# Kernel optimization log

Hardware: AMD Instinct MI355X
Metric: run time of the kernel (lower is better)

The kernel has to match this reference:

```python
import jax, jax.numpy as jnp
import numpy as np

B, L, C, D, H, EL, DFF, NC, PH = 32, 512, 64, 512, 8, 3, 2048, 8, 256
DK = D // H


def _ln(x, g, b):
    m = jnp.mean(x, -1, keepdims=True)
    v = jnp.var(x, -1, keepdims=True)
    return (x - m) / jnp.sqrt(v + 1e-5) * g + b


def _projector(x, stats, cw, w1, b1, w2, b2, w3):
    # circular Conv1d over feature axis with seq_len input channels -> 1 channel
    xp = jnp.pad(x, ((0, 0), (0, 0), (1, 1)), mode='wrap')  # [B,L,C+2]
    win = jnp.stack([xp[:, :, :-2], xp[:, :, 1:-1], xp[:, :, 2:]], -1)  # [B,L,C,3]
    y = jnp.einsum('bsck,sk->bc', win, cw)  # [B,C]
    h = jnp.concatenate([y, stats[:, 0, :]], -1)  # [B,2C]
    h = jax.nn.relu(h @ w1.T + b1)
    h = jax.nn.relu(h @ w2.T + b2)
    return h @ w3.T


def setup_inputs() -> dict:
    key = jax.random.key(0)
    ks = jax.random.split(key, 20)
    n = lambda i, shape, s=0.02: jax.random.normal(ks[i], shape, jnp.float32) * s
    return {
        'x_enc': jax.random.normal(ks[0], (B, L, C), jnp.float32),
        'emb_conv_w': n(1, (D, C, 3), 0.05),
        'tau_conv_w': n(2, (L, 3), 0.05),
        'tau_w1': n(3, (PH, 2 * C)), 'tau_b1': jnp.zeros((PH,), jnp.float32),
        'tau_w2': n(4, (PH, PH)), 'tau_b2': jnp.zeros((PH,), jnp.float32),
        'tau_w3': n(5, (1, PH)),
        'delta_conv_w': n(6, (L, 3), 0.05),
        'delta_w1': n(7, (PH, 2 * C)), 'delta_b1': jnp.zeros((PH,), jnp.float32),
        'delta_w2': n(8, (PH, PH)), 'delta_b2': jnp.zeros((PH,), jnp.float32),
        'delta_w3': n(9, (L, PH)),
        'Wq': n(10, (EL, D, D)), 'bq': jnp.zeros((EL, D), jnp.float32),
        'Wk': n(11, (EL, D, D)), 'bk': jnp.zeros((EL, D), jnp.float32),
        'Wv': n(12, (EL, D, D)), 'bv': jnp.zeros((EL, D), jnp.float32),
        'Wo': n(13, (EL, D, D)), 'bo': jnp.zeros((EL, D), jnp.float32),
        'ff_w1': n(14, (EL, DFF, D)), 'ff_b1': jnp.zeros((EL, DFF), jnp.float32),
        'ff_w2': n(15, (EL, D, DFF)), 'ff_b2': jnp.zeros((EL, D), jnp.float32),
        'ln1_g': jnp.ones((EL, D), jnp.float32), 'ln1_b': jnp.zeros((EL, D), jnp.float32),
        'ln2_g': jnp.ones((EL, D), jnp.float32), 'ln2_b': jnp.zeros((EL, D), jnp.float32),
        'norm_g': jnp.ones((D,), jnp.float32), 'norm_b': jnp.zeros((D,), jnp.float32),
        'proj_w': n(16, (NC, D * L), 0.005), 'proj_b': jnp.zeros((NC,), jnp.float32),
    }


def reference(x_enc, emb_conv_w, tau_conv_w, tau_w1, tau_b1, tau_w2, tau_b2, tau_w3,
              delta_conv_w, delta_w1, delta_b1, delta_w2, delta_b2, delta_w3,
              Wq, bq, Wk, bk, Wv, bv, Wo, bo, ff_w1, ff_b1, ff_w2, ff_b2,
              ln1_g, ln1_b, ln2_g, ln2_b, norm_g, norm_b, proj_w, proj_b):
    x_raw = jax.lax.stop_gradient(x_enc)
    mean_enc = jax.lax.stop_gradient(jnp.mean(x_enc, 1, keepdims=True))  # [B,1,C]
    std_enc = jax.lax.stop_gradient(jnp.sqrt(jnp.var(x_enc, axis=1, keepdims=True) + 1e-5))
    tau = jnp.exp(_projector(x_raw, std_enc, tau_conv_w, tau_w1, tau_b1, tau_w2, tau_b2, tau_w3))  # [B,1]
    delta = _projector(x_raw, mean_enc, delta_conv_w, delta_w1, delta_b1, delta_w2, delta_b2, delta_w3)  # [B,L]

    # TokenEmbedding: circular Conv1d (kernel 3, no bias) over time + sinusoidal PE
    xp = jnp.pad(x_enc, ((0, 0), (1, 1), (0, 0)), mode='wrap')
    win = jnp.stack([xp[:, :-2], xp[:, 1:-1], xp[:, 2:]], -1)  # [B,L,C,3]
    x = jnp.einsum('blck,dck->bld', win, emb_conv_w)
    pos = jnp.arange(L, dtype=jnp.float32)[:, None]
    div = jnp.exp(jnp.arange(0, D, 2, dtype=jnp.float32) * (-jnp.log(10000.0) / D))
    pe = jnp.zeros((L, D), jnp.float32).at[:, 0::2].set(jnp.sin(pos * div)).at[:, 1::2].set(jnp.cos(pos * div))
    x = x + pe[None]

    scale = 1.0 / jnp.sqrt(jnp.float32(DK))
    tau4 = tau[:, :, None, None]      # [B,1,1,1]
    delta4 = delta[:, None, None, :]  # [B,1,1,S]
    for i in range(EL):
        q = (x @ Wq[i].T + bq[i]).reshape(B, L, H, DK)
        k = (x @ Wk[i].T + bk[i]).reshape(B, L, H, DK)
        v = (x @ Wv[i].T + bv[i]).reshape(B, L, H, DK)
        scores = jnp.einsum('blhe,bshe->bhls', q, k) * tau4 + delta4  # DSAttention rescale/shift
        A = jax.nn.softmax(scale * scores, axis=-1)
        o = jnp.einsum('bhls,bshd->blhd', A, v).reshape(B, L, D)
        x = x + (o @ Wo[i].T + bo[i])
        x = _ln(x, ln1_g[i], ln1_b[i])
        y = jax.nn.gelu(x @ ff_w1[i].T + ff_b1[i], approximate=False)  # conv1 kernel=1 == linear
        y = y @ ff_w2[i].T + ff_b2[i]
        x = _ln(x + y, ln2_g[i], ln2_b[i])
    x = _ln(x, norm_g, norm_b)
    out = jax.nn.gelu(x, approximate=False).reshape(B, -1)
    return out @ proj_w.T + proj_b
```

## Files before the change

### kernel.cpp

```cpp
#include <hip/hip_runtime.h>
#include <hip/hip_bf16.h>
#include <math.h>

#define B_   32
#define L_   512
#define C_   64
#define D_   512
#define H_   8
#define EL_  3
#define DFF_ 2048
#define NC_  8
#define PH_  256
#define DK_  64
#define NTOK (B_*L_)

typedef unsigned short u16;
typedef unsigned int   u32;
typedef __attribute__((ext_vector_type(4))) float f32x4;
typedef __attribute__((ext_vector_type(8))) short s16x8;

__device__ __forceinline__ u16 f2b(float f){
  u32 u = __float_as_uint(f);
  u32 r = (u + 0x7fffu + ((u >> 16) & 1u)) >> 16;
  return (u16)r;
}
__device__ __forceinline__ float b2f(u16 u){ return __uint_as_float(((u32)u) << 16); }

__device__ __forceinline__ void gload16(const void* g, void* l){
  __builtin_amdgcn_global_load_lds(
      (const __attribute__((address_space(1))) u32*)g,
      (__attribute__((address_space(3))) u32*)l, 16, 0, 0);
}

__device__ __forceinline__ float gelu_exact(float x){
  return 0.5f * x * (1.f + erff(x * 0.70710678118654752f));
}


__global__ __launch_bounds__(256) void k_stats(const float* __restrict__ x,
    float* __restrict__ mean, float* __restrict__ stdv){
  int b = blockIdx.x, t = threadIdx.x;
  const float* p = x + (size_t)b*L_*C_;
  float s = 0.f, q = 0.f;
  for (int i = t; i < L_*C_; i += 256){ float v = p[i]; s += v; q += v*v; }
  __shared__ float ss[256], qq[256];
  ss[t] = s; qq[t] = q;
  __syncthreads();
  if (t < 64){
    float S = ss[t]+ss[t+64]+ss[t+128]+ss[t+192];
    float Q = qq[t]+qq[t+64]+qq[t+128]+qq[t+192];
    float m = S*(1.f/L_);
    mean[b*64+t] = m;
    stdv[b*64+t] = sqrtf(Q*(1.f/L_) - m*m + 1e-5f);
  }
}

__global__ __launch_bounds__(256) void k_mlp(const float* __restrict__ x,
    const float* __restrict__ mean, const float* __restrict__ stdv,
    const float* __restrict__ cw_t, const float* __restrict__ w1t, const float* __restrict__ b1t,
    const float* __restrict__ w2t, const float* __restrict__ b2t, const float* __restrict__ w3t,
    const float* __restrict__ cw_d, const float* __restrict__ w1d, const float* __restrict__ b1d,
    const float* __restrict__ w2d, const float* __restrict__ b2d, const float* __restrict__ w3d,
    float* __restrict__ tau, float* __restrict__ delta)
{
  int b = blockIdx.x, sel = blockIdx.y, t = threadIdx.x;
  const float* cw = sel ? cw_d : cw_t;
  const float* w1 = sel ? w1d : w1t;  const float* b1 = sel ? b1d : b1t;
  const float* w2 = sel ? w2d : w2t;  const float* b2 = sel ? b2d : b2t;
  const float* st = sel ? mean : stdv;
  __shared__ float h0[128], h1s[256], h2s[256], red[256];
  __shared__ float c4[4][64];
  {
    int c = t & 63, g = t >> 6;
    int cm = (c+63)&63, cp = (c+1)&63;
    const float* xrow = x + (size_t)b*L_*C_;
    float acc = 0.f;
    for (int s = g*128; s < (g+1)*128; ++s){
      const float* r = xrow + s*C_;
      acc += r[cm]*cw[s*3] + r[c]*cw[s*3+1] + r[cp]*cw[s*3+2];
    }
    c4[g][c] = acc;
  }
  __syncthreads();
  if (t < 64)       h0[t] = c4[0][t]+c4[1][t]+c4[2][t]+c4[3][t];
  else if (t < 128) h0[t] = st[b*64 + (t-64)];
  __syncthreads();
  { float a = b1[t]; for (int j=0;j<128;++j) a += h0[j]*w1[t*128+j]; h1s[t] = fmaxf(a,0.f); }
  __syncthreads();
  { float a = b2[t]; for (int j=0;j<256;++j) a += h1s[j]*w2[t*256+j]; h2s[t] = fmaxf(a,0.f); }
  __syncthreads();
  if (sel == 0){
    red[t] = h2s[t]*w3t[t];
    __syncthreads();
    for (int o=128;o>0;o>>=1){ if (t<o) red[t]+=red[t+o]; __syncthreads(); }
    if (t == 0) tau[b] = expf(red[0]);
  } else {
    for (int l = t; l < L_; l += 256){
      float a = 0.f;
      for (int j=0;j<256;++j) a += h2s[j]*w3d[l*256+j];
      delta[b*L_ + l] = a;
    }
  }
}

__global__ void k_pe(float* __restrict__ pe){
  int i = blockIdx.x*256 + threadIdx.x;
  if (i >= L_*D_/2) return;
  int l = i >> 8, j = i & 255;
  float div = expf((float)(2*j) * (-9.210340371976184f / (float)D_));
  float arg = (float)l * div;
  pe[l*D_ + 2*j]   = sinf(arg);
  pe[l*D_ + 2*j+1] = cosf(arg);
}

__global__ void k_awin(const float* __restrict__ x, u16* __restrict__ awin){
  int i = blockIdx.x*256 + threadIdx.x;
  if (i >= NTOK*192) return;
  int col = i % 192, row = i / 192;
  int k = col >> 6, c = col & 63;
  int b = row >> 9, l = row & 511;
  int ls = (l + k + 511) & 511;
  awin[i] = f2b(x[((size_t)((b<<9) | ls))*64 + c]);
}

__global__ void k_embw(const float* __restrict__ w, u16* __restrict__ o){
  int i = blockIdx.x*256 + threadIdx.x;
  if (i >= D_*192) return;
  int d = i / 192, col = i % 192, k = col >> 6, c = col & 63;
  o[i] = f2b(w[(d*64 + c)*3 + k]);
}

__global__ void k_packqkv(const float* __restrict__ Wq, const float* __restrict__ Wk,
                          const float* __restrict__ Wv, u16* __restrict__ o){
  int i = blockIdx.x*256 + threadIdx.x;
  if (i >= EL_*1536*D_) return;
  int e = i / (1536*D_), r = i % (1536*D_);
  int n = r / D_, k = r % D_;
  const float* src = (n < 512) ? Wq + ((size_t)e*512 + n)*512 + k
                   : (n < 1024) ? Wk + ((size_t)e*512 + (n-512))*512 + k
                                : Wv + ((size_t)e*512 + (n-1024))*512 + k;
  o[i] = f2b(*src);
}
__global__ void k_packb(const float* __restrict__ bq, const float* __restrict__ bk,
                        const float* __restrict__ bv, float* __restrict__ o){
  int i = blockIdx.x*256 + threadIdx.x;
  if (i >= EL_*1536) return;
  int e = i/1536, n = i%1536;
  o[i] = (n<512) ? bq[e*512+n] : (n<1024) ? bk[e*512+n-512] : bv[e*512+n-1024];
}

__global__ void k_f2b(const float* __restrict__ in, u16* __restrict__ out, int n){
  int i = blockIdx.x*256 + threadIdx.x;
  if (i < n) out[i] = f2b(in[i]);
}

__global__ __launch_bounds__(256,2) void k_gemm(
    const u16* __restrict__ A, const u16* __restrict__ Bm,
    int M, int N, int K,
    const float* __restrict__ bias, const float* __restrict__ pe,
    int dogelu,
    float* __restrict__ outF, u16* __restrict__ outB)
{
  __shared__ u16 As[128*64];
  __shared__ u16 Bs[128*64];
  int tid = threadIdx.x;
  int l = tid & 63, w = tid >> 6;
  int wr = w >> 1, wc = w & 1;
  int lo = l & 15, lg = l >> 4;

  int flat = blockIdx.x + gridDim.x*blockIdx.y;
  int nwg  = gridDim.x*gridDim.y;
  int n1   = ((nwg & 7) == 0) ? ((flat & 7)*(nwg >> 3) + (flat >> 3)) : flat;
  int bx   = n1 % gridDim.x, by = n1 / gridDim.x;
  int m0 = by * 128, n0 = bx * 128;

  f32x4 acc[4][4];
  #pragma unroll
  for (int m=0;m<4;++m)
    #pragma unroll
    for (int n=0;n<4;++n) acc[m][n] = (f32x4){0.f,0.f,0.f,0.f};

  int swz = lo & 7;
  int ktn = K >> 6;
  for (int kt = 0; kt < ktn; ++kt){
    #pragma unroll
    for (int i=0;i<4;++i){
      int cA = i*256 + tid;
      int row = cA >> 3, sub = (cA & 7) ^ (row & 7);
      gload16(A  + (size_t)(m0+row)*K + kt*64 + sub*8, &As[cA*8]);
      gload16(Bm + (size_t)(n0+row)*K + kt*64 + sub*8, &Bs[cA*8]);
    }
    __syncthreads();
    #pragma unroll
    for (int kk=0;kk<2;++kk){
      int cb = ((kk<<2)|lg) ^ swz;
      s16x8 af[4], bfr[4];
      #pragma unroll
      for (int m=0;m<4;++m) af[m]  = *(const s16x8*)&As[(wr*64 + m*16 + lo)*64 + cb*8];
      #pragma unroll
      for (int n=0;n<4;++n) bfr[n] = *(const s16x8*)&Bs[(wc*64 + n*16 + lo)*64 + cb*8];
      #pragma unroll
      for (int m=0;m<4;++m)
        #pragma unroll
        for (int n=0;n<4;++n)
          acc[m][n] = __builtin_amdgcn_mfma_f32_16x16x32_bf16(af[m], bfr[n], acc[m][n], 0,0,0);
    }
    __syncthreads();
  }

  #pragma unroll
  for (int m=0;m<4;++m){
    int rbase = m0 + wr*64 + m*16 + lg*4;
    #pragma unroll
    for (int n=0;n<4;++n){
      int col = n0 + wc*64 + n*16 + lo;
      float bv = bias ? bias[col] : 0.f;
      #pragma unroll
      for (int r=0;r<4;++r){
        int row = rbase + r;
        float v = acc[m][n][r] + bv;
        if (pe) v += pe[(size_t)(row & 511)*N + col];
        if (dogelu) v = gelu_exact(v);
        size_t o = (size_t)row*N + col;
        if (outF) outF[o] = v;
        if (outB) outB[o] = f2b(v);
      }
    }
  }
}

__global__ __launch_bounds__(512,2) void k_gemm256(
    const u16* __restrict__ A, const u16* __restrict__ Bm,
    int M, int N, int K,
    const float* __restrict__ bias,
    int dogelu,
    float* __restrict__ outF, u16* __restrict__ outB)
{
  __shared__ u16 AS[2][256*64];
  __shared__ u16 BS[2][256*64];
  int tid = threadIdx.x;
  int l = tid & 63, w = tid >> 6;
  int wr = w >> 2, wc = w & 3;
  int lo = l & 15, lg = l >> 4;
  int swz = lo & 7;

  int flat = blockIdx.x + gridDim.x*blockIdx.y;
  int nwg  = gridDim.x*gridDim.y;
  int n1   = ((nwg & 7) == 0) ? ((flat & 7)*(nwg >> 3) + (flat >> 3)) : flat;
  int bx   = n1 % gridDim.x, by = n1 / gridDim.x;
  int m0 = by * 256, n0 = bx * 256;

  f32x4 acc[8][4];
  #pragma unroll
  for (int m=0;m<8;++m)
    #pragma unroll
    for (int n=0;n<4;++n) acc[m][n] = (f32x4){0.f,0.f,0.f,0.f};

  auto STAGE = [&](int buf, int kt){
    #pragma unroll
    for (int i=0;i<4;++i){
      int c = i*512 + tid;
      int row = c >> 3, sub = (c & 7) ^ (row & 7);
      gload16(A  + (size_t)(m0+row)*K + kt*64 + sub*8, &AS[buf][c*8]);
      gload16(Bm + (size_t)(n0+row)*K + kt*64 + sub*8, &BS[buf][c*8]);
    }
  };

  STAGE(0, 0);
  __syncthreads();

  int ktn = K >> 6;
  for (int kt = 0; kt < ktn; ++kt){
    int cur = kt & 1;
    if (kt + 1 < ktn) STAGE(cur^1, kt+1);
    const u16* Ac = &AS[cur][0];
    const u16* Bc = &BS[cur][0];

    #pragma unroll
    for (int q=0;q<4;++q){
      int qm = q >> 1, qn = q & 1;
      s16x8 af[4][2], bf2[2][2];
      #pragma unroll
      for (int mm=0;mm<4;++mm)
        #pragma unroll
        for (int ks=0;ks<2;++ks){
          int row = wr*128 + (qm*4+mm)*16 + lo;
          int cb  = ((ks<<2)|lg) ^ swz;
          af[mm][ks] = *(const s16x8*)&Ac[row*64 + cb*8];
        }
      #pragma unroll
      for (int nn=0;nn<2;++nn)
        #pragma unroll
        for (int ks=0;ks<2;++ks){
          int row = wc*64 + (qn*2+nn)*16 + lo;
          int cb  = ((ks<<2)|lg) ^ swz;
          bf2[nn][ks] = *(const s16x8*)&Bc[row*64 + cb*8];
        }
      __builtin_amdgcn_s_setprio(1);
      #pragma unroll
      for (int mm=0;mm<4;++mm)
        #pragma unroll
        for (int nn=0;nn<2;++nn)
          #pragma unroll
          for (int ks=0;ks<2;++ks)
            acc[qm*4+mm][qn*2+nn] = __builtin_amdgcn_mfma_f32_16x16x32_bf16(
                af[mm][ks], bf2[nn][ks], acc[qm*4+mm][qn*2+nn], 0,0,0);
      __builtin_amdgcn_s_setprio(0);
      __builtin_amdgcn_sched_barrier(0);
    }
    __syncthreads();
  }

  #pragma unroll
  for (int m=0;m<8;++m){
    int rbase = m0 + wr*128 + m*16 + lg*4;
    #pragma unroll
    for (int n=0;n<4;++n){
      int col = n0 + wc*64 + n*16 + lo;
      float bv = bias ? bias[col] : 0.f;
      #pragma unroll
      for (int r=0;r<4;++r){
        int row = rbase + r;
        float v = acc[m][n][r] + bv;
        if (dogelu) v = gelu_exact(v);
        size_t o = (size_t)row*N + col;
        if (outF) outF[o] = v;
        if (outB) outB[o] = f2b(v);
      }
    }
  }
}

__global__ __launch_bounds__(256) void k_vt(const u16* __restrict__ qkv, u16* __restrict__ vT){
  int st = blockIdx.x, h = blockIdx.y, b = blockIdx.z;
  __shared__ u16 tile[64][72];
  int t = threadIdx.x;
  int r = t >> 2, q = t & 3;
  const u16* src = qkv + ((size_t)(b*L_ + st*64 + r))*1536 + 1024 + h*64 + q*16;
  #pragma unroll
  for (int j=0;j<16;++j) tile[r][q*16+j] = src[j];
  __syncthreads();
  u16* dst = vT + (((size_t)(b*H_ + h))*64 + r)*L_ + st*64 + q*16;
  #pragma unroll
  for (int j=0;j<16;++j) dst[j] = tile[q*16+j][r];
}

__global__ __launch_bounds__(256) void k_attn(
    const u16* __restrict__ qkv, const u16* __restrict__ vT,
    const float* __restrict__ tau, const float* __restrict__ delta,
    u16* __restrict__ obf)
{
  __shared__ u16 Ks[2][64*64];
  __shared__ u16 Vs[2][64*64];
  __shared__ u16 plds[4][16*64];
  int id = blockIdx.x;
  int qt = id >> 8, hb = id & 255, h = hb >> 5, b = hb & 31;
  int tid = threadIdx.x, l = tid & 63, w = tid >> 6;
  int lo = l & 15, lg = l >> 4;
  int q0 = qt*64 + w*16;

  const u16* qrow = qkv + ((size_t)(b*L_ + q0 + lo))*1536 + h*64;
  s16x8 qf0 = *(const s16x8*)(qrow + lg*8);
  s16x8 qf1 = *(const s16x8*)(qrow + 32 + lg*8);

  const u16* Kg = qkv + (size_t)b*L_*1536 + 512 + h*64;
  const u16* Vg = vT + ((size_t)(b*H_ + h))*64*L_;

  float taus = tau[b] * 0.125f;
  f32x4 oacc[4];
  #pragma unroll
  for (int n=0;n<4;++n) oacc[n] = (f32x4){0.f,0.f,0.f,0.f};
  float mrow[4] = {-3e38f,-3e38f,-3e38f,-3e38f};
  float lrow[4] = {0.f,0.f,0.f,0.f};
  const float* dptr = delta + b*L_;
  u16* pw = &plds[w][0];

  auto STAGE = [&](int buf, int s0){
    #pragma unroll
    for (int i=0;i<2;++i){
      int c = i*256 + tid;
      int row = c >> 3, sub = (c & 7) ^ (row & 7);
      gload16(Kg + (size_t)(s0 + row)*1536 + sub*8, &Ks[buf][c*8]);
      gload16(Vg + (size_t)row*L_ + s0 + sub*8,     &Vs[buf][c*8]);
    }
  };

  STAGE(0, 0);
  __syncthreads();

  int swz = lo & 7;
  for (int it = 0; it < 8; ++it){
    int s0 = it*64, cur = it & 1;
    if (it < 7) STAGE(cur^1, s0 + 64);
    const u16* Kc = &Ks[cur][0];
    const u16* Vc = &Vs[cur][0];

    f32x4 sacc[4];
    #pragma unroll
    for (int t2=0;t2<4;++t2) sacc[t2] = (f32x4){0.f,0.f,0.f,0.f};
    #pragma unroll
    for (int kk=0;kk<2;++kk){
      #pragma unroll
      for (int t2=0;t2<4;++t2){
        s16x8 kf = *(const s16x8*)&Kc[(t2*16 + lo)*64 + (((kk*4 + lg) ^ swz)*8)];
        sacc[t2] = __builtin_amdgcn_mfma_f32_16x16x32_bf16(kk ? qf1 : qf0, kf, sacc[t2], 0,0,0);
      }
    }

    float p[4][4];
    float rm[4] = {-3e38f,-3e38f,-3e38f,-3e38f};
    #pragma unroll
    for (int t2=0;t2<4;++t2){
      float dl = dptr[s0 + t2*16 + lo] * 0.125f;
      #pragma unroll
      for (int r=0;r<4;++r){
        float sc = taus*sacc[t2][r] + dl;
        p[t2][r] = sc;
        rm[r] = fmaxf(rm[r], sc);
      }
    }
    #pragma unroll
    for (int r=0;r<4;++r){
      #pragma unroll
      for (int off=1; off<16; off<<=1) rm[r] = fmaxf(rm[r], __shfl_xor(rm[r], off));
    }
    float alpha[4];
    #pragma unroll
    for (int r=0;r<4;++r){
      float mn = fmaxf(mrow[r], rm[r]);
      alpha[r] = __expf(mrow[r] - mn);
      mrow[r] = mn;
      float acc = 0.f;
      #pragma unroll
      for (int t2=0;t2<4;++t2){ p[t2][r] = __expf(p[t2][r] - mn); acc += p[t2][r]; }
      #pragma unroll
      for (int off=1; off<16; off<<=1) acc += __shfl_xor(acc, off);
      lrow[r] = lrow[r]*alpha[r] + acc;
    }
    #pragma unroll
    for (int n=0;n<4;++n)
      #pragma unroll
      for (int r=0;r<4;++r) oacc[n][r] *= alpha[r];

    #pragma unroll
    for (int t2=0;t2<4;++t2)
      #pragma unroll
      for (int r=0;r<4;++r){
        int q = lg*4 + r;
        int cb = (t2*2 + (lo>>3)) ^ (q & 7);
        pw[q*64 + cb*8 + (lo & 7)] = f2b(p[t2][r]);
      }
    asm volatile("" ::: "memory");
    #pragma unroll
    for (int kk=0;kk<2;++kk){
      s16x8 pa = *(const s16x8*)&pw[lo*64 + (((kk*4 + lg) ^ swz)*8)];
      #pragma unroll
      for (int n=0;n<4;++n){
        s16x8 vf = *(const s16x8*)&Vc[(n*16 + lo)*64 + (((kk*4 + lg) ^ swz)*8)];
        oacc[n] = __builtin_amdgcn_mfma_f32_16x16x32_bf16(pa, vf, oacc[n], 0,0,0);
      }
    }
    __syncthreads();
  }

  float inv[4];
  #pragma unroll
  for (int r=0;r<4;++r) inv[r] = 1.f / lrow[r];
  #pragma unroll
  for (int n=0;n<4;++n)
    #pragma unroll
    for (int r=0;r<4;++r){
      int row = q0 + lg*4 + r;
      int col = h*64 + n*16 + lo;
      obf[((size_t)(b*L_ + row))*512 + col] = f2b(oacc[n][r]*inv[r]);
    }
}

__global__ __launch_bounds__(256) void k_ln(const float* __restrict__ X, const float* __restrict__ R,
    const float* __restrict__ gw, const float* __restrict__ bw,
    float* __restrict__ outF, u16* __restrict__ outB, int dogelu)
{
  int l = threadIdx.x & 63, w = threadIdx.x >> 6;
  size_t row = (size_t)blockIdx.x*4 + w;
  const float4* x4 = (const float4*)(X + row*D_);
  float4 a0 = x4[l*2], a1 = x4[l*2+1];
  if (R){
    const float4* r4 = (const float4*)(R + row*D_);
    float4 c0 = r4[l*2], c1 = r4[l*2+1];
    a0.x+=c0.x; a0.y+=c0.y; a0.z+=c0.z; a0.w+=c0.w;
    a1.x+=c1.x; a1.y+=c1.y; a1.z+=c1.z; a1.w+=c1.w;
  }
  float v[8] = {a0.x,a0.y,a0.z,a0.w,a1.x,a1.y,a1.z,a1.w};
  float s = 0.f, q = 0.f;
  #pragma unroll
  for (int j=0;j<8;++j){ s += v[j]; q += v[j]*v[j]; }
  #pragma unroll
  for (int off=1; off<64; off<<=1){ s += __shfl_xor(s, off); q += __shfl_xor(q, off); }
  float mean = s * (1.f/D_);
  float var  = q * (1.f/D_) - mean*mean;
  float rstd = rsqrtf(var + 1e-5f);
  int c0i = l*8;
  #pragma unroll
  for (int j=0;j<8;++j){
    int c = c0i + j;
    float t = (v[j] - mean)*rstd*gw[c] + bw[c];
    if (dogelu) t = gelu_exact(t);
    if (outF) outF[row*D_ + c] = t;
    if (outB) outB[row*D_ + c] = f2b(t);
  }
}

__global__ __launch_bounds__(256) void k_proj1(const float* __restrict__ g, const float* __restrict__ pw,
    float* __restrict__ pp)
{
  int b = blockIdx.x, nc = blockIdx.y, kc = blockIdx.z, t = threadIdx.x;
  const float4* g4 = (const float4*)(g  + (size_t)b*(L_*D_) + (size_t)kc*32768);
  const float4* w4 = (const float4*)(pw + (size_t)nc*(L_*D_) + (size_t)kc*32768);
  float acc = 0.f;
  for (int k = t; k < 8192; k += 256){
    float4 a = g4[k], c = w4[k];
    acc += a.x*c.x + a.y*c.y + a.z*c.z + a.w*c.w;
  }
  #pragma unroll
  for (int off=1; off<64; off<<=1) acc += __shfl_xor(acc, off);
  __shared__ float red[4];
  if ((t & 63) == 0) red[t>>6] = acc;
  __syncthreads();
  if (t == 0) pp[((b*NC_ + nc)<<3) + kc] = red[0]+red[1]+red[2]+red[3];
}
__global__ void k_proj2(const float* __restrict__ pp, const float* __restrict__ pb,
                        float* __restrict__ out){
  int t = threadIdx.x;
  float s = 0.f;
  #pragma unroll
  for (int k=0;k<8;++k) s += pp[t*8 + k];
  out[t] = s + pb[t & 7];
}

extern "C" void kernel_launch(void* const* d_in, const int* in_sizes, int n_in,
                              void* d_out, int out_size, void* d_ws, size_t ws_size,
                              hipStream_t stream)
{
  const float* x_enc        = (const float*)d_in[0];
  const float* emb_conv_w   = (const float*)d_in[1];
  const float* tau_conv_w   = (const float*)d_in[2];
  const float* tau_w1       = (const float*)d_in[3];
  const float* tau_b1       = (const float*)d_in[4];
  const float* tau_w2       = (const float*)d_in[5];
  const float* tau_b2       = (const float*)d_in[6];
  const float* tau_w3       = (const float*)d_in[7];
  const float* delta_conv_w = (const float*)d_in[8];
  const float* delta_w1     = (const float*)d_in[9];
  const float* delta_b1     = (const float*)d_in[10];
  const float* delta_w2     = (const float*)d_in[11];
  const float* delta_b2     = (const float*)d_in[12];
  const float* delta_w3     = (const float*)d_in[13];
  const float* Wq  = (const float*)d_in[14];
  const float* bq  = (const float*)d_in[15];
  const float* Wk  = (const float*)d_in[16];
  const float* bk  = (const float*)d_in[17];
  const float* Wv  = (const float*)d_in[18];
  const float* bv  = (const float*)d_in[19];
  const float* Wo  = (const float*)d_in[20];
  const float* bo  = (const float*)d_in[21];
  const float* ff_w1 = (const float*)d_in[22];
  const float* ff_b1 = (const float*)d_in[23];
  const float* ff_w2 = (const float*)d_in[24];
  const float* ff_b2 = (const float*)d_in[25];
  const float* ln1_g = (const float*)d_in[26];
  const float* ln1_b = (const float*)d_in[27];
  const float* ln2_g = (const float*)d_in[28];
  const float* ln2_b = (const float*)d_in[29];
  const float* norm_g = (const float*)d_in[30];
  const float* norm_b = (const float*)d_in[31];
  const float* proj_w = (const float*)d_in[32];
  const float* proj_b = (const float*)d_in[33];
  (void)in_sizes; (void)n_in; (void)out_size; (void)ws_size;

  char* ws = (char*)d_ws;
  size_t off = 0;
  auto alloc = [&](size_t n){ size_t o = off; off += (n + 255) & ~(size_t)255; return o; };
  float* xf    = (float*)(ws + alloc((size_t)NTOK*512*4));
  u16*   xb    = (u16*)  (ws + alloc((size_t)NTOK*512*2));
  char*  U     =          ws + alloc((size_t)NTOK*2048*2);
  u16*   qkv   = (u16*)U;
  u16*   h1    = (u16*)U;
  u16*   awin  = (u16*)U;
  u16*   obf   = (u16*)(U + (size_t)NTOK*1536*2);
  u16*   vT    = (u16*)  (ws + alloc((size_t)NTOK*512*2));
  float* tmp   = (float*)(ws + alloc((size_t)NTOK*512*4));
  float* pe    = (float*)(ws + alloc((size_t)512*512*4));
  u16*   WqkvB = (u16*)  (ws + alloc((size_t)EL_*1536*512*2));
  u16*   WoB   = (u16*)  (ws + alloc((size_t)EL_*512*512*2));
  u16*   W1B   = (u16*)  (ws + alloc((size_t)EL_*2048*512*2));
  u16*   W2B   = (u16*)  (ws + alloc((size_t)EL_*512*2048*2));
  u16*   embB  = (u16*)  (ws + alloc((size_t)512*192*2));
  float* bqkv  = (float*)(ws + alloc((size_t)EL_*1536*4));
  float* meanb = (float*)(ws + alloc(2048*4));
  float* stdb  = (float*)(ws + alloc(2048*4));
  float* taub  = (float*)(ws + alloc(256));
  float* deltab= (float*)(ws + alloc((size_t)B_*512*4));
  float* pp    = (float*)(ws + alloc((size_t)B_*NC_*8*4));

  k_packqkv<<<(EL_*1536*512+255)/256, 256, 0, stream>>>(Wq, Wk, Wv, WqkvB);
  k_packb  <<<(EL_*1536+255)/256,     256, 0, stream>>>(bq, bk, bv, bqkv);
  k_f2b    <<<(EL_*512*512+255)/256,  256, 0, stream>>>(Wo, WoB, EL_*512*512);
  k_f2b    <<<(EL_*2048*512+255)/256, 256, 0, stream>>>(ff_w1, W1B, EL_*2048*512);
  k_f2b    <<<(EL_*512*2048+255)/256, 256, 0, stream>>>(ff_w2, W2B, EL_*512*2048);
  k_embw   <<<(D_*192+255)/256,       256, 0, stream>>>(emb_conv_w, embB);

  k_stats<<<B_, 256, 0, stream>>>(x_enc, meanb, stdb);
  k_mlp<<<dim3(B_,2), 256, 0, stream>>>(x_enc, meanb, stdb,
      tau_conv_w, tau_w1, tau_b1, tau_w2, tau_b2, tau_w3,
      delta_conv_w, delta_w1, delta_b1, delta_w2, delta_b2, delta_w3,
      taub, deltab);
  k_pe  <<<(L_*D_/2+255)/256, 256, 0, stream>>>(pe);
  k_awin<<<(NTOK*192+255)/256, 256, 0, stream>>>(x_enc, awin);

  k_gemm<<<dim3(4,128), 256, 0, stream>>>(awin, embB, NTOK, 512, 192, nullptr, pe, 0, xf, xb);

  for (int e = 0; e < EL_; ++e){
    k_gemm256<<<dim3(6,64), 512, 0, stream>>>(xb, WqkvB + (size_t)e*1536*512, NTOK, 1536, 512,
                                              bqkv + e*1536, 0, nullptr, qkv);
    k_vt  <<<dim3(8,8,32), 256, 0, stream>>>(qkv, vT);
    k_attn<<<2048, 256, 0, stream>>>(qkv, vT, taub, deltab, obf);
    k_gemm<<<dim3(4,128), 256, 0, stream>>>(obf, WoB + (size_t)e*512*512, NTOK, 512, 512,
                                            bo + e*512, nullptr, 0, tmp, nullptr);
    k_ln  <<<NTOK/4, 256, 0, stream>>>(xf, tmp, ln1_g + e*512, ln1_b + e*512, xf, xb, 0);
    k_gemm256<<<dim3(8,64), 512, 0, stream>>>(xb, W1B + (size_t)e*2048*512, NTOK, 2048, 512,
                                              ff_b1 + e*2048, 1, nullptr, h1);
    k_gemm<<<dim3(4,128), 256, 0, stream>>>(h1, W2B + (size_t)e*512*2048, NTOK, 512, 2048,
                                            ff_b2 + e*512, nullptr, 0, tmp, nullptr);
    k_ln  <<<NTOK/4, 256, 0, stream>>>(xf, tmp, ln2_g + e*512, ln2_b + e*512, xf,
                                       (e == EL_-1) ? nullptr : xb, 0);
  }

  k_ln   <<<NTOK/4, 256, 0, stream>>>(xf, nullptr, norm_g, norm_b, tmp, nullptr, 1);
  k_proj1<<<dim3(B_,NC_,8), 256, 0, stream>>>(tmp, proj_w, pp);
  k_proj2<<<1, 256, 0, stream>>>(pp, proj_b, (float*)d_out);
}
```

Measured before the change: 1.496 ms.

## Replace 256-tile GEMM with triple-buffered 128-tile pipelined GEMM kernel

Swaps the double-buffered 256x256 GEMM for a 128x128-tile kernel with a three-stage LDS ring. Loads run two k-tiles ahead and are waited on with explicit vmcnt counts and raw s_barriers. The new kernel serves the QKV, FFN1 and FFN2 GEMMs, so FFN2 also leaves the old k_gemm. Launch bounds on k_gemm and k_attn are raised to request four waves per SIMD, which trades register budget for occupancy and may cause spills.

```diff
diff --git a/kernel.cpp b/kernel.cpp
--- a/kernel.cpp
+++ b/kernel.cpp
@@ -154,7 +154,7 @@
   if (i < n) out[i] = f2b(in[i]);
 }
 
-__global__ __launch_bounds__(256,2) void k_gemm(
+__global__ __launch_bounds__(256,4) void k_gemm(
     const u16* __restrict__ A, const u16* __restrict__ Bm,
     int M, int N, int K,
     const float* __restrict__ bias, const float* __restrict__ pe,
@@ -229,18 +229,17 @@
   }
 }
 
-__global__ __launch_bounds__(512,2) void k_gemm256(
+__global__ __launch_bounds__(256) void k_gemmP(
     const u16* __restrict__ A, const u16* __restrict__ Bm,
     int M, int N, int K,
-    const float* __restrict__ bias,
-    int dogelu,
+    const float* __restrict__ bias, int dogelu,
     float* __restrict__ outF, u16* __restrict__ outB)
 {
-  __shared__ u16 AS[2][256*64];
-  __shared__ u16 BS[2][256*64];
+  __shared__ u16 As[3][128*64];
+  __shared__ u16 Bs[3][128*64];
   int tid = threadIdx.x;
   int l = tid & 63, w = tid >> 6;
-  int wr = w >> 2, wc = w & 3;
+  int wr = w >> 1, wc = w & 1;
   int lo = l & 15, lg = l >> 4;
   int swz = lo & 7;
 
@@ -248,72 +247,80 @@
   int nwg  = gridDim.x*gridDim.y;
   int n1   = ((nwg & 7) == 0) ? ((flat & 7)*(nwg >> 3) + (flat >> 3)) : flat;
   int bx   = n1 % gridDim.x, by = n1 / gridDim.x;
-  int m0 = by * 256, n0 = bx * 256;
-
-  f32x4 acc[8][4];
-  #pragma unroll
-  for (int m=0;m<8;++m)
+  int m0 = by * 128, n0 = bx * 128;
+
+  const u16* srcA[4]; const u16* srcB[4];
+  #pragma unroll
+  for (int i=0;i<4;++i){
+    int c = i*256 + tid;
+    int row = c >> 3, sub = (c & 7) ^ (row & 7);
+    srcA[i] = A  + (size_t)(m0+row)*K + sub*8;
+    srcB[i] = Bm + (size_t)(n0+row)*K + sub*8;
+  }
+
+  f32x4 acc[4][4];
+  #pragma unroll
+  for (int m=0;m<4;++m)
     #pragma unroll
     for (int n=0;n<4;++n) acc[m][n] = (f32x4){0.f,0.f,0.f,0.f};
 
   auto STAGE = [&](int buf, int kt){
     #pragma unroll
     for (int i=0;i<4;++i){
-      int c = i*512 + tid;
-      int row = c >> 3, sub = (c & 7) ^ (row & 7);
-      gload16(A  + (size_t)(m0+row)*K + kt*64 + sub*8, &AS[buf][c*8]);
-      gload16(Bm + (size_t)(n0+row)*K + kt*64 + sub*8, &BS[buf][c*8]);
+      gload16(srcA[i] + kt*64, &As[buf][(i*256+tid)*8]);
+      gload16(srcB[i] + kt*64, &Bs[buf][(i*256+tid)*8]);
     }
   };
-
+  auto COMPUTE = [&](int buf){
+    const u16* Ac = &As[buf][0];
+    const u16* Bc = &Bs[buf][0];
+    #pragma unroll
+    for (int kk=0;kk<2;++kk){
+      int cb = ((kk<<2)|lg) ^ swz;
+      s16x8 af[4], bfr[4];
+      #pragma unroll
+      for (int m=0;m<4;++m) af[m]  = *(const s16x8*)&Ac[(wr*64 + m*16 + lo)*64 + cb*8];
+      #pragma unroll
+      for (int n=0;n<4;++n) bfr[n] = *(const s16x8*)&Bc[(wc*64 + n*16 + lo)*64 + cb*8];
+      #pragma unroll
+      for (int m=0;m<4;++m)
+        #pragma unroll
+        for (int n=0;n<4;++n)
+          acc[m][n] = __builtin_amdgcn_mfma_f32_16x16x32_bf16(af[m], bfr[n], acc[m][n], 0,0,0);
+    }
+  };
+
+  int ktn = K >> 6;
   STAGE(0, 0);
-  __syncthreads();
-
-  int ktn = K >> 6;
-  for (int kt = 0; kt < ktn; ++kt){
-    int cur = kt & 1;
-    if (kt + 1 < ktn) STAGE(cur^1, kt+1);
-    const u16* Ac = &AS[cur][0];
-    const u16* Bc = &BS[cur][0];
-
-    #pragma unroll
-    for (int q=0;q<4;++q){
-      int qm = q >> 1, qn = q & 1;
-      s16x8 af[4][2], bf2[2][2];
-      #pragma unroll
-      for (int mm=0;mm<4;++mm)
-        #pragma unroll
-        for (int ks=0;ks<2;++ks){
-          int row = wr*128 + (qm*4+mm)*16 + lo;
-          int cb  = ((ks<<2)|lg) ^ swz;
-          af[mm][ks] = *(const s16x8*)&Ac[row*64 + cb*8];
-        }
-      #pragma unroll
-      for (int nn=0;nn<2;++nn)
-        #pragma unroll
-        for (int ks=0;ks<2;++ks){
-          int row = wc*64 + (qn*2+nn)*16 + lo;
-          int cb  = ((ks<<2)|lg) ^ swz;
-          bf2[nn][ks] = *(const s16x8*)&Bc[row*64 + cb*8];
-        }
-      __builtin_amdgcn_s_setprio(1);
-      #pragma unroll
-      for (int mm=0;mm<4;++mm)
-        #pragma unroll
-        for (int nn=0;nn<2;++nn)
-          #pragma unroll
-          for (int ks=0;ks<2;++ks)
-            acc[qm*4+mm][qn*2+nn] = __builtin_amdgcn_mfma_f32_16x16x32_bf16(
-                af[mm][ks], bf2[nn][ks], acc[qm*4+mm][qn*2+nn], 0,0,0);
-      __builtin_amdgcn_s_setprio(0);
-      __builtin_amdgcn_sched_barrier(0);
-    }
-    __syncthreads();
-  }
-
-  #pragma unroll
-  for (int m=0;m<8;++m){
-    int rbase = m0 + wr*128 + m*16 + lg*4;
+  STAGE(1, 1);
+
+  int k = 0;
+  for (; k < ktn-2; ++k){
+    STAGE((k+2)%3, k+2);
+    asm volatile("s_waitcnt vmcnt(16)" ::: "memory");
+    __builtin_amdgcn_sched_barrier(0);
+    __builtin_amdgcn_s_barrier();
+    __builtin_amdgcn_sched_barrier(0);
+    COMPUTE(k%3);
+    __builtin_amdgcn_sched_barrier(0);
+    __builtin_amdgcn_s_barrier();
+  }
+  asm volatile("s_waitcnt vmcnt(8)" ::: "memory");
+  __builtin_amdgcn_sched_barrier(0);
+  __builtin_amdgcn_s_barrier();
+  __builtin_amdgcn_sched_barrier(0);
+  COMPUTE((ktn-2)%3);
+  __builtin_amdgcn_sched_barrier(0);
+  __builtin_amdgcn_s_barrier();
+  asm volatile("s_waitcnt vmcnt(0)" ::: "memory");
+  __builtin_amdgcn_sched_barrier(0);
+  __builtin_amdgcn_s_barrier();
+  __builtin_amdgcn_sched_barrier(0);
+  COMPUTE((ktn-1)%3);
+
+  #pragma unroll
+  for (int m=0;m<4;++m){
+    int rbase = m0 + wr*64 + m*16 + lg*4;
     #pragma unroll
     for (int n=0;n<4;++n){
       int col = n0 + wc*64 + n*16 + lo;
@@ -345,7 +352,7 @@
   for (int j=0;j<16;++j) dst[j] = tile[q*16+j][r];
 }
 
-__global__ __launch_bounds__(256) void k_attn(
+__global__ __launch_bounds__(256,4) void k_attn(
     const u16* __restrict__ qkv, const u16* __restrict__ vT,
     const float* __restrict__ tau, const float* __restrict__ delta,
     u16* __restrict__ obf)
@@ -620,17 +627,17 @@
   k_gemm<<<dim3(4,128), 256, 0, stream>>>(awin, embB, NTOK, 512, 192, nullptr, pe, 0, xf, xb);
 
   for (int e = 0; e < EL_; ++e){
-    k_gemm256<<<dim3(6,64), 512, 0, stream>>>(xb, WqkvB + (size_t)e*1536*512, NTOK, 1536, 512,
+    k_gemmP<<<dim3(12,128), 256, 0, stream>>>(xb, WqkvB + (size_t)e*1536*512, NTOK, 1536, 512,
                                               bqkv + e*1536, 0, nullptr, qkv);
     k_vt  <<<dim3(8,8,32), 256, 0, stream>>>(qkv, vT);
     k_attn<<<2048, 256, 0, stream>>>(qkv, vT, taub, deltab, obf);
     k_gemm<<<dim3(4,128), 256, 0, stream>>>(obf, WoB + (size_t)e*512*512, NTOK, 512, 512,
                                             bo + e*512, nullptr, 0, tmp, nullptr);
     k_ln  <<<NTOK/4, 256, 0, stream>>>(xf, tmp, ln1_g + e*512, ln1_b + e*512, xf, xb, 0);
-    k_gemm256<<<dim3(8,64), 512, 0, stream>>>(xb, W1B + (size_t)e*2048*512, NTOK, 2048, 512,
+    k_gemmP<<<dim3(16,128), 256, 0, stream>>>(xb, W1B + (size_t)e*2048*512, NTOK, 2048, 512,
                                               ff_b1 + e*2048, 1, nullptr, h1);
-    k_gemm<<<dim3(4,128), 256, 0, stream>>>(h1, W2B + (size_t)e*512*2048, NTOK, 512, 2048,
-                                            ff_b2 + e*512, nullptr, 0, tmp, nullptr);
+    k_gemmP<<<dim3(4,128), 256, 0, stream>>>(h1, W2B + (size_t)e*512*2048, NTOK, 512, 2048,
+                                             ff_b2 + e*512, 0, tmp, nullptr);
     k_ln  <<<NTOK/4, 256, 0, stream>>>(xf, tmp, ln2_g + e*512, ln2_b + e*512, xf,
                                        (e == EL_-1) ? nullptr : xb, 0);
   }
```

Result: slower. 1.774 ms (+18.6%).
